# Optimization experiments

Hardware: AMD Instinct MI355X
Metric: run time of the kernel (lower is better)

The kernel has to match this reference:

```python
import jax, jax.numpy as jnp
import numpy as np

B, IDF, CDF, IH, IW, SRC = 32, 1024, 1024, 48, 48, 256


def setup_inputs() -> dict:
    key = jax.random.key(0)
    k1, k2, k3, k4 = jax.random.split(key, 4)
    inp = {
        "input": jax.random.normal(k1, (B, IDF, IH, IW), dtype=jnp.float32),
        "context": jax.random.normal(k2, (B, CDF, SRC), dtype=jnp.float32),
        "mask": jax.random.randint(k3, (B, SRC), 0, 2).astype(bool) & jax.random.randint(k4, (B, SRC), 0, 2).astype(bool),
        "W": jax.random.normal(jax.random.fold_in(key, 7), (IDF, CDF), dtype=jnp.float32) * 0.02,
    }
    return inp


def reference(input, context, mask, W):
    b, idf, ih, iw = input.shape
    q = ih * iw
    s = context.shape[2]
    # conv1x1(cdf->idf) on context: pure channel matmul
    sourceT = jnp.einsum("ic,bcs->bis", W, context)            # [B, idf, S]
    target = input.reshape(b, idf, q)                            # [B, idf, Q]
    attn = jnp.einsum("biq,bis->bqs", target, sourceT)          # [B, Q, S]
    attn_flat = attn.reshape(b * q, s)
    # faithful to original: mask.repeat(queryL, 1) tiles batch-major mask
    # onto batch-major-flattened rows -> row i uses mask[i % B]
    mask_full = jnp.tile(mask, (q, 1))                           # [Q*B, S] == [B*Q, S]
    attn_flat = jnp.where(mask_full, -jnp.inf, attn_flat)
    attn_flat = jax.nn.softmax(attn_flat, axis=-1)
    attn = attn_flat.reshape(b, q, s)
    attnT = jnp.transpose(attn, (0, 2, 1))                       # [B, S, Q]
    weightedContext = jnp.einsum("bis,bsq->biq", sourceT, attnT)
    weightedContext = weightedContext.reshape(b, idf, ih, iw)
    attn_out = attnT.reshape(b, s, ih, iw)
    return weightedContext, attn_out
```

## Files before the change

### kernel.cpp

```cpp
#include <hip/hip_runtime.h>

#define Bn  32
#define IDF 1024
#define CDF 1024
#define Qn  2304
#define Sn  256

typedef _Float16 f16;
typedef _Float16 f16x2 __attribute__((ext_vector_type(2)));
typedef _Float16 f16x4 __attribute__((ext_vector_type(4)));
typedef _Float16 f16x8 __attribute__((ext_vector_type(8)));
typedef float    f32x4 __attribute__((ext_vector_type(4)));

__device__ __forceinline__ void gll16(const void* g, void* l) {
    __builtin_amdgcn_global_load_lds((const __attribute__((address_space(1))) void*)g,
                                     (__attribute__((address_space(3))) void*)l, 16, 0, 0);
}

__device__ __forceinline__ void fsplit(float x, f16& hi, f16& lo) {
    hi = (f16)x;
    lo = (f16)(x - (float)hi);
}

__global__ __launch_bounds__(256) void k_wsplit(const float* __restrict__ W,
                                                f16* __restrict__ Wh, f16* __restrict__ Wl) {
    const int idx = (blockIdx.x * 256 + threadIdx.x) * 4;
    const float4 v = *reinterpret_cast<const float4*>(&W[idx]);
    f16x4 h4, l4;
    f16 h, l;
    fsplit(v.x, h, l); h4[0] = h; l4[0] = l;
    fsplit(v.y, h, l); h4[1] = h; l4[1] = l;
    fsplit(v.z, h, l); h4[2] = h; l4[2] = l;
    fsplit(v.w, h, l); h4[3] = h; l4[3] = l;
    *reinterpret_cast<f16x4*>(&Wh[idx]) = h4;
    *reinterpret_cast<f16x4*>(&Wl[idx]) = l4;
}

__global__ __launch_bounds__(256) void k_srcT(const f16* __restrict__ Wh,
                                              const f16* __restrict__ Wl,
                                              const float* __restrict__ ctx,
                                              f16* __restrict__ si_h, f16* __restrict__ si_l,
                                              f16* __restrict__ is_h, f16* __restrict__ is_l) {
    __shared__ alignas(16) char smem[49152];
    const int tid = threadIdx.x;
    const int w = tid >> 6, lane = tid & 63, g = lane >> 4, l15 = lane & 15;
    const int rxor = ((l15 >> 1) & 3) << 4;

    const int lin = (blockIdx.z * 8 + blockIdx.y) * 2 + blockIdx.x;
    const int swz = (lin & 7) * 64 + (lin >> 3);
    const int b = swz >> 4, rr = swz & 15;
    const int i0 = (rr >> 1) * 128, s0 = (rr & 1) * 128;

    const float* Cp = ctx + (size_t)b * CDF * Sn + s0;
    const int sl = tid & 127, ch = tid >> 7;
    const int swzw = ((sl >> 1) & 3) << 4;

    f32x4 acc[2][8];
    {
        f32x4 z = {0.f, 0.f, 0.f, 0.f};
        #pragma unroll
        for (int mf = 0; mf < 2; ++mf)
            #pragma unroll
            for (int nf = 0; nf < 8; ++nf)
                acc[mf][nf] = z;
    }

    #pragma unroll
    for (int part = 0; part < 2; ++part) {
        const int byt = w * 2048 + part * 1024 + lane * 16;
        const int rw = byt >> 6;
        const int co = ((((byt >> 4) & 3) ^ ((rw >> 1) & 3)) << 3);
        const size_t go = (size_t)(i0 + rw) * CDF + co;
        gll16(Wh + go, smem + w * 2048 + part * 1024);
        gll16(Wl + go, smem + 8192 + w * 2048 + part * 1024);
    }
    {
        float cv[16];
        #pragma unroll
        for (int j = 0; j < 16; ++j)
            cv[j] = Cp[(size_t)(ch * 16 + j) * Sn + sl];
        f16x8 h0, h1, l0, l1;
        #pragma unroll
        for (int j = 0; j < 8; ++j) { f16 h, l; fsplit(cv[j], h, l); h0[j] = h; l0[j] = l; }
        #pragma unroll
        for (int j = 0; j < 8; ++j) { f16 h, l; fsplit(cv[8 + j], h, l); h1[j] = h; l1[j] = l; }
        char* cb = smem + 16384 + sl * 64;
        *reinterpret_cast<f16x8*>(cb + (((ch * 32) + 0) ^ swzw))        = h0;
        *reinterpret_cast<f16x8*>(cb + (((ch * 32) + 16) ^ swzw))       = h1;
        *reinterpret_cast<f16x8*>(cb + 8192 + (((ch * 32) + 0) ^ swzw)) = l0;
        *reinterpret_cast<f16x8*>(cb + 8192 + (((ch * 32) + 16) ^ swzw))= l1;
    }
    __syncthreads();

    for (int t = 0; t < 32; ++t) {
        const int kk = t * 32;
        f16x8 fwh[2], fwl[2];
        #pragma unroll
        for (int mf = 0; mf < 2; ++mf) {
            const int row = w * 32 + mf * 16 + l15;
            fwh[mf] = *reinterpret_cast<const f16x8*>(smem + row * 64 + ((g * 16) ^ rxor));
            fwl[mf] = *reinterpret_cast<const f16x8*>(smem + 8192 + row * 64 + ((g * 16) ^ rxor));
        }
        asm volatile("s_waitcnt lgkmcnt(0)" ::: "memory");
        __builtin_amdgcn_sched_barrier(0);
        float cv[16];
        if (t < 31) {
            #pragma unroll
            for (int part = 0; part < 2; ++part) {
                const int byt = w * 2048 + part * 1024 + lane * 16;
                const int rw = byt >> 6;
                const int co = ((((byt >> 4) & 3) ^ ((rw >> 1) & 3)) << 3);
                const size_t go = (size_t)(i0 + rw) * CDF + kk + 32 + co;
                gll16(Wh + go, smem + w * 2048 + part * 1024);
                gll16(Wl + go, smem + 8192 + w * 2048 + part * 1024);
            }
            #pragma unroll
            for (int j = 0; j < 16; ++j)
                cv[j] = Cp[(size_t)(kk + 32 + ch * 16 + j) * Sn + sl];
        }
        const char* cbuf = smem + 16384 + (t & 1) * 16384;
        __builtin_amdgcn_s_setprio(1);
        #pragma unroll
        for (int nf = 0; nf < 8; ++nf) {
            const int srow = nf * 16 + l15;
            const f16x8 fch = *reinterpret_cast<const f16x8*>(cbuf + srow * 64 + ((g * 16) ^ rxor));
            const f16x8 fcl = *reinterpret_cast<const f16x8*>(cbuf + 8192 + srow * 64 + ((g * 16) ^ rxor));
            #pragma unroll
            for (int mf = 0; mf < 2; ++mf) {
                acc[mf][nf] = __builtin_amdgcn_mfma_f32_16x16x32_f16(fwh[mf], fch, acc[mf][nf], 0, 0, 0);
                acc[mf][nf] = __builtin_amdgcn_mfma_f32_16x16x32_f16(fwh[mf], fcl, acc[mf][nf], 0, 0, 0);
                acc[mf][nf] = __builtin_amdgcn_mfma_f32_16x16x32_f16(fwl[mf], fch, acc[mf][nf], 0, 0, 0);
            }
        }
        __builtin_amdgcn_s_setprio(0);
        if (t < 31) {
            f16x8 h0, h1, l0, l1;
            #pragma unroll
            for (int j = 0; j < 8; ++j) { f16 h, l; fsplit(cv[j], h, l); h0[j] = h; l0[j] = l; }
            #pragma unroll
            for (int j = 0; j < 8; ++j) { f16 h, l; fsplit(cv[8 + j], h, l); h1[j] = h; l1[j] = l; }
            char* cb = smem + 16384 + ((t + 1) & 1) * 16384 + sl * 64;
            *reinterpret_cast<f16x8*>(cb + (((ch * 32) + 0) ^ swzw))        = h0;
            *reinterpret_cast<f16x8*>(cb + (((ch * 32) + 16) ^ swzw))       = h1;
            *reinterpret_cast<f16x8*>(cb + 8192 + (((ch * 32) + 0) ^ swzw)) = l0;
            *reinterpret_cast<f16x8*>(cb + 8192 + (((ch * 32) + 16) ^ swzw))= l1;
        }
        __syncthreads();
    }

    #pragma unroll
    for (int mf = 0; mf < 2; ++mf)
        #pragma unroll
        for (int nf = 0; nf < 8; ++nf) {
            f16x4 h4, l4;
            #pragma unroll
            for (int r = 0; r < 4; ++r) { f16 h, l; fsplit(acc[mf][nf][r], h, l); h4[r] = h; l4[r] = l; }
            const int s  = s0 + nf * 16 + l15;
            const int ib = i0 + w * 32 + mf * 16 + g * 4;
            const size_t so = ((size_t)b * Sn + s) * IDF + ib;
            *reinterpret_cast<f16x4*>(&si_h[so]) = h4;
            *reinterpret_cast<f16x4*>(&si_l[so]) = l4;
        }

    #pragma unroll
    for (int p = 0; p < 2; ++p) {
        __syncthreads();
        #pragma unroll
        for (int mf = 0; mf < 2; ++mf) {
            const int ibase = w * 32 + mf * 16 + g * 4;
            #pragma unroll
            for (int nf4 = 0; nf4 < 4; ++nf4) {
                const int sl2 = nf4 * 16 + l15;
                #pragma unroll
                for (int r = 0; r < 4; ++r) {
                    const int row = ibase + r;
                    const int byo = (sl2 * 2) ^ ((row & 7) << 4);
                    f16 h, l; fsplit(acc[mf][p * 4 + nf4][r], h, l);
                    *reinterpret_cast<f16*>(smem + row * 128 + byo) = h;
                    *reinterpret_cast<f16*>(smem + 16384 + row * 128 + byo) = l;
                }
            }
        }
        __syncthreads();
        #pragma unroll
        for (int k = 0; k < 4; ++k) {
            const int c = tid + 256 * k;
            const int row = c >> 3, sc = (c & 7) * 8;
            const int byo = (sc * 2) ^ ((row & 7) << 4);
            const f16x8 vh = *reinterpret_cast<const f16x8*>(smem + row * 128 + byo);
            const f16x8 vl = *reinterpret_cast<const f16x8*>(smem + 16384 + row * 128 + byo);
            const size_t o = ((size_t)b * IDF + i0 + row) * Sn + s0 + p * 64 + sc;
            *reinterpret_cast<f16x8*>(&is_h[o]) = vh;
            *reinterpret_cast<f16x8*>(&is_l[o]) = vl;
        }
    }
}

__global__ __launch_bounds__(256) void k_attn(const float* __restrict__ inp,
                                              const f16* __restrict__ si_h,
                                              const f16* __restrict__ si_l,
                                              const int* __restrict__ mask,
                                              float* __restrict__ out1,
                                              f16* __restrict__ Ph) {
    __shared__ alignas(16) char smem[49152];
    const int tid = threadIdx.x;
    const int w = tid >> 6, lane = tid & 63, g = lane >> 4, l15 = lane & 15;
    const int rxor = ((l15 >> 1) & 3) << 4;
    const int awz  = ((lane >> 1) & 3) << 4;

    const int lin = blockIdx.y * 36 + blockIdx.x;
    const int swzb = (lin & 7) * 144 + (lin >> 3);
    const int b = swzb / 36, qt = swzb - b * 36;
    const int q0 = qt * 64;

    const float* Ap = inp + (size_t)b * IDF * Qn + q0;
    const f16* BhG = si_h + (size_t)b * Sn * IDF;
    const f16* BlG = si_l + (size_t)b * Sn * IDF;

    f32x4 acc[4][4];
    {
        f32x4 z = {0.f, 0.f, 0.f, 0.f};
        #pragma unroll
        for (int mf = 0; mf < 4; ++mf)
            #pragma unroll
            for (int nf = 0; nf < 4; ++nf)
                acc[mf][nf] = z;
    }

    #pragma unroll
    for (int it = 0; it < 4; ++it) {
        const int byt = w * 4096 + it * 1024 + lane * 16;
        const int s = byt >> 6;
        const int ko = ((((byt >> 4) & 3) ^ ((s >> 1) & 3)) << 3);
        const size_t go = (size_t)s * IDF + ko;
        gll16(BhG + go, smem + 16384 + w * 4096 + it * 1024);
        gll16(BlG + go, smem + 32768 + w * 4096 + it * 1024);
    }
    {
        float av[8];
        #pragma unroll
        for (int j = 0; j < 8; ++j)
            av[j] = Ap[(size_t)(w * 8 + j) * Qn + lane];
        f16x8 ah, al;
        #pragma unroll
        for (int j = 0; j < 8; ++j) { f16 h, lo; fsplit(av[j], h, lo); ah[j] = h; al[j] = lo; }
        *reinterpret_cast<f16x8*>(smem + lane * 64 + ((w * 16) ^ awz)) = ah;
        *reinterpret_cast<f16x8*>(smem + 4096 + lane * 64 + ((w * 16) ^ awz)) = al;
    }
    __syncthreads();

    for (int t = 0; t < 32; ++t) {
        const int kk = t * 32;
        f16x8 fbh[4], fbl[4];
        #pragma unroll
        for (int nf = 0; nf < 4; ++nf) {
            const int row = w * 64 + nf * 16 + l15;
            fbh[nf] = *reinterpret_cast<const f16x8*>(smem + 16384 + row * 64 + ((g * 16) ^ rxor));
            fbl[nf] = *reinterpret_cast<const f16x8*>(smem + 32768 + row * 64 + ((g * 16) ^ rxor));
        }
        asm volatile("s_waitcnt lgkmcnt(0)" ::: "memory");
        __builtin_amdgcn_sched_barrier(0);
        float av[8];
        if (t < 31) {
            #pragma unroll
            for (int it = 0; it < 4; ++it) {
                const int byt = w * 4096 + it * 1024 + lane * 16;
                const int s = byt >> 6;
                const int ko = ((((byt >> 4) & 3) ^ ((s >> 1) & 3)) << 3);
                const size_t go = (size_t)s * IDF + kk + 32 + ko;
                gll16(BhG + go, smem + 16384 + w * 4096 + it * 1024);
                gll16(BlG + go, smem + 32768 + w * 4096 + it * 1024);
            }
            #pragma unroll
            for (int j = 0; j < 8; ++j)
                av[j] = Ap[(size_t)(kk + 32 + w * 8 + j) * Qn + lane];
        }
        const char* ab = smem + (t & 1) * 8192;
        __builtin_amdgcn_s_setprio(1);
        #pragma unroll
        for (int mf = 0; mf < 4; ++mf) {
            const f16x8 fah = *reinterpret_cast<const f16x8*>(ab + (mf * 16 + l15) * 64 + ((g * 16) ^ rxor));
            const f16x8 fal = *reinterpret_cast<const f16x8*>(ab + 4096 + (mf * 16 + l15) * 64 + ((g * 16) ^ rxor));
            #pragma unroll
            for (int nf = 0; nf < 4; ++nf) {
                acc[mf][nf] = __builtin_amdgcn_mfma_f32_16x16x32_f16(fah, fbh[nf], acc[mf][nf], 0, 0, 0);
                acc[mf][nf] = __builtin_amdgcn_mfma_f32_16x16x32_f16(fah, fbl[nf], acc[mf][nf], 0, 0, 0);
                acc[mf][nf] = __builtin_amdgcn_mfma_f32_16x16x32_f16(fal, fbh[nf], acc[mf][nf], 0, 0, 0);
            }
        }
        __builtin_amdgcn_s_setprio(0);
        if (t < 31) {
            f16x8 ah, al;
            #pragma unroll
            for (int j = 0; j < 8; ++j) { f16 h, lo; fsplit(av[j], h, lo); ah[j] = h; al[j] = lo; }
            char* wb = smem + ((t + 1) & 1) * 8192;
            *reinterpret_cast<f16x8*>(wb + lane * 64 + ((w * 16) ^ awz)) = ah;
            *reinterpret_cast<f16x8*>(wb + 4096 + lane * 64 + ((w * 16) ^ awz)) = al;
        }
        __syncthreads();
    }

    int mv[2][4][4];
    #pragma unroll
    for (int h2 = 0; h2 < 2; ++h2)
        #pragma unroll
        for (int r = 0; r < 4; ++r)
            #pragma unroll
            for (int nf = 0; nf < 4; ++nf)
                mv[h2][r][nf] = mask[(h2 * 16 + g * 4 + r) * Sn + w * 64 + nf * 16 + l15];

    float* redm = reinterpret_cast<float*>(smem + 34816);
    float* reds = reinterpret_cast<float*>(smem + 35840);

    float mx[4][4], sm[4][4];
    #pragma unroll
    for (int mf = 0; mf < 4; ++mf)
        #pragma unroll
        for (int r = 0; r < 4; ++r) {
            float m = -3.0e38f;
            #pragma unroll
            for (int nf = 0; nf < 4; ++nf)
                if (!mv[mf & 1][r][nf]) m = fmaxf(m, acc[mf][nf][r]);
            m = fmaxf(m, __shfl_xor(m, 1, 64));
            m = fmaxf(m, __shfl_xor(m, 2, 64));
            m = fmaxf(m, __shfl_xor(m, 4, 64));
            m = fmaxf(m, __shfl_xor(m, 8, 64));
            mx[mf][r] = m;
        }
    if (l15 == 0) {
        #pragma unroll
        for (int mf = 0; mf < 4; ++mf)
            #pragma unroll
            for (int r = 0; r < 4; ++r)
                redm[w * 64 + mf * 16 + g * 4 + r] = mx[mf][r];
    }
    __syncthreads();
    #pragma unroll
    for (int mf = 0; mf < 4; ++mf)
        #pragma unroll
        for (int r = 0; r < 4; ++r) {
            const int q = mf * 16 + g * 4 + r;
            const float gm = fmaxf(fmaxf(redm[q], redm[64 + q]), fmaxf(redm[128 + q], redm[192 + q]));
            float ssum = 0.f;
            #pragma unroll
            for (int nf = 0; nf < 4; ++nf) {
                const float p = mv[mf & 1][r][nf] ? 0.f : __expf(acc[mf][nf][r] - gm);
                acc[mf][nf][r] = p;
                ssum += p;
            }
            ssum += __shfl_xor(ssum, 1, 64);
            ssum += __shfl_xor(ssum, 2, 64);
            ssum += __shfl_xor(ssum, 4, 64);
            ssum += __shfl_xor(ssum, 8, 64);
            sm[mf][r] = ssum;
        }
    if (l15 == 0) {
        #pragma unroll
        for (int mf = 0; mf < 4; ++mf)
            #pragma unroll
            for (int r = 0; r < 4; ++r)
                reds[w * 64 + mf * 16 + g * 4 + r] = sm[mf][r];
    }
    __syncthreads();
    #pragma unroll
    for (int mf = 0; mf < 4; ++mf)
        #pragma unroll
        for (int r = 0; r < 4; ++r) {
            const int q = mf * 16 + g * 4 + r;
            const float inv = 1.0f / (reds[q] + reds[64 + q] + reds[128 + q] + reds[192 + q]);
            #pragma unroll
            for (int nf = 0; nf < 4; ++nf)
                acc[mf][nf][r] *= inv;
        }

    float* Pl = reinterpret_cast<float*>(smem);
    float* O1 = out1 + (size_t)b * Sn * Qn + q0;
    f16* PhB = Ph + ((size_t)b * Qn + q0) * Sn;
    #pragma unroll
    for (int hf = 0; hf < 2; ++hf) {
        __syncthreads();
        if ((w >> 1) == hf) {
            #pragma unroll
            for (int mf = 0; mf < 4; ++mf)
                #pragma unroll
                for (int nf = 0; nf < 4; ++nf)
                    *reinterpret_cast<f32x4*>(
                        &Pl[((w & 1) * 64 + nf * 16 + l15) * 68 + mf * 16 + g * 4]) = acc[mf][nf];
        }
        __syncthreads();
        #pragma unroll
        for (int j = 0; j < 8; ++j) {
            const int sr = (tid >> 4) + j * 16;
            const int u  = (tid & 15) * 4;
            const f32x4 v = *reinterpret_cast<const f32x4*>(&Pl[sr * 68 + u]);
            *reinterpret_cast<f32x4*>(&O1[(size_t)(hf * 128 + sr) * Qn + u]) = v;
        }
        #pragma unroll
        for (int j = 0; j < 16; ++j) {
            const int colU = l15 + 16 * (j & 3);
            const int q    = (w * 4 + g) + 16 * (j >> 2);
            const float p0 = Pl[(2 * colU) * 68 + q];
            const float p1 = Pl[(2 * colU + 1) * 68 + q];
            f16x2 hh; hh[0] = (f16)p0; hh[1] = (f16)p1;
            *reinterpret_cast<f16x2*>(&PhB[(size_t)q * Sn + hf * 128 + 2 * colU]) = hh;
        }
    }
}

__global__ __launch_bounds__(256) void k_wc(const f16* __restrict__ is_h,
                                            const f16* __restrict__ is_l,
                                            const f16* __restrict__ Ph,
                                            float* __restrict__ out0) {
    __shared__ alignas(16) char smem[49152];
    const int tid = threadIdx.x;
    const int w = tid >> 6, lane = tid & 63, g = lane >> 4, l15 = lane & 15;
    const int wi = w >> 1, wq = w & 1;
    const int rxor = ((l15 >> 1) & 3) << 4;

    const int lin = (blockIdx.z * 8 + blockIdx.y) * 18 + blockIdx.x;
    const int swz = (lin & 7) * 576 + (lin >> 3);
    const int b = swz / 144;
    const int rr = swz - b * 144;
    const int it = rr / 18, qt = rr - it * 18;
    const int i0 = it * 128, q0 = qt * 128;

    const f16* AhG = is_h + ((size_t)b * IDF + i0) * Sn;
    const f16* AlG = is_l + ((size_t)b * IDF + i0) * Sn;
    const f16* BG  = Ph  + ((size_t)b * Qn + q0) * Sn;

    f32x4 acc[4][4];
    {
        f32x4 z = {0.f, 0.f, 0.f, 0.f};
        #pragma unroll
        for (int mf = 0; mf < 4; ++mf)
            #pragma unroll
            for (int nf = 0; nf < 4; ++nf)
                acc[mf][nf] = z;
    }

    #pragma unroll
    for (int t2 = 0; t2 < 2; ++t2) {
        const int byt = (w * 2 + t2) * 1024 + lane * 16;
        const int rw = byt >> 6;
        const int so = ((((byt >> 4) & 3) ^ ((rw >> 1) & 3)) << 3);
        const size_t go = (size_t)rw * Sn + so;
        gll16(AhG + go, smem + (w * 2 + t2) * 1024);
        gll16(AlG + go, smem + 8192 + (w * 2 + t2) * 1024);
        gll16(BG  + go, smem + 16384 + (w * 2 + t2) * 1024);
    }
    __syncthreads();

    for (int t = 0; t < 8; ++t) {
        const int kk = t * 32;
        if (t < 7) {
            #pragma unroll
            for (int t2 = 0; t2 < 2; ++t2) {
                const int byt = (w * 2 + t2) * 1024 + lane * 16;
                const int rw = byt >> 6;
                const int so = ((((byt >> 4) & 3) ^ ((rw >> 1) & 3)) << 3);
                const size_t go = (size_t)rw * Sn + kk + 32 + so;
                char* dst = smem + ((t + 1) & 1) * 24576 + (w * 2 + t2) * 1024;
                gll16(AhG + go, dst);
                gll16(AlG + go, dst + 8192);
                gll16(BG  + go, dst + 16384);
            }
        }
        const char* buf = smem + (t & 1) * 24576;
        f16x8 fah[4], fal[4];
        #pragma unroll
        for (int mf = 0; mf < 4; ++mf) {
            const int row = wi * 64 + mf * 16 + l15;
            fah[mf] = *reinterpret_cast<const f16x8*>(buf + row * 64 + ((g * 16) ^ rxor));
            fal[mf] = *reinterpret_cast<const f16x8*>(buf + 8192 + row * 64 + ((g * 16) ^ rxor));
        }
        __builtin_amdgcn_s_setprio(1);
        #pragma unroll
        for (int nf = 0; nf < 4; ++nf) {
            const int row = wq * 64 + nf * 16 + l15;
            const f16x8 fbh = *reinterpret_cast<const f16x8*>(buf + 16384 + row * 64 + ((g * 16) ^ rxor));
            #pragma unroll
            for (int mf = 0; mf < 4; ++mf) {
                acc[mf][nf] = __builtin_amdgcn_mfma_f32_16x16x32_f16(fah[mf], fbh, acc[mf][nf], 0, 0, 0);
                acc[mf][nf] = __builtin_amdgcn_mfma_f32_16x16x32_f16(fal[mf], fbh, acc[mf][nf], 0, 0, 0);
            }
        }
        __builtin_amdgcn_s_setprio(0);
        __syncthreads();
    }
    float* O = out0 + ((size_t)b * IDF + i0 + wi * 64) * Qn + q0 + wq * 64;
    #pragma unroll
    for (int mf = 0; mf < 4; ++mf)
        #pragma unroll
        for (int nf = 0; nf < 4; ++nf)
            #pragma unroll
            for (int r = 0; r < 4; ++r)
                O[(size_t)(mf * 16 + g * 4 + r) * Qn + nf * 16 + l15] = acc[mf][nf][r];
}

extern "C" void kernel_launch(void* const* d_in, const int* in_sizes, int n_in,
                              void* d_out, int out_size, void* d_ws, size_t ws_size,
                              hipStream_t stream) {
    const float* inp  = (const float*)d_in[0];
    const float* ctx  = (const float*)d_in[1];
    const int*   mask = (const int*)  d_in[2];
    const float* W    = (const float*)d_in[3];
    float* out0 = (float*)d_out;
    float* out1 = out0 + (size_t)Bn * IDF * Qn;

    char* ws = (char*)d_ws;
    const size_t SZ = (size_t)Bn * Sn * IDF * sizeof(f16);
    f16* si_h = (f16*)(ws);
    f16* si_l = (f16*)(ws + SZ);
    f16* is_h = (f16*)(ws + 2 * SZ);
    f16* is_l = (f16*)(ws + 3 * SZ);
    f16* Ph   = (f16*)(ws + 4 * SZ);
    f16* Wh   = (f16*)(ws + 4 * SZ);
    f16* Wl   = Wh + (size_t)IDF * CDF;

    hipLaunchKernelGGL(k_wsplit, dim3(IDF * CDF / 1024), dim3(256), 0, stream, W, Wh, Wl);
    hipLaunchKernelGGL(k_srcT, dim3(Sn / 128, IDF / 128, Bn), dim3(256), 0, stream,
                       Wh, Wl, ctx, si_h, si_l, is_h, is_l);
    hipLaunchKernelGGL(k_attn, dim3(Qn / 64, Bn), dim3(256), 0, stream,
                       inp, si_h, si_l, mask, out1, Ph);
    hipLaunchKernelGGL(k_wc, dim3(Qn / 128, IDF / 128, Bn), dim3(256), 0, stream,
                       is_h, is_l, Ph, out0);
}
```

Before: 396.0 us.

## Double query tile in attention kernel to reuse source tiles across more rows

Each attention block now covers 128 query positions instead of 64. Every staged tile of the split fp16 source matrix therefore feeds 8 MFMA row fragments instead of 4, halving global and LDS traffic for the source operand per query. The input load is restructured so 128 threads each split 16 channel values into hi/lo halves, with LDS grown to 64KB, launch bounds set to 2 blocks per CU, and the softmax reductions and epilogue writes re-indexed for the larger tile. The trade-offs are more accumulator registers, half as many blocks in the grid, and lower occupancy.

New measurement: 386.0 us. -2.5%, faster.

```diff
diff --git a/kernel.cpp b/kernel.cpp
--- a/kernel.cpp
+++ b/kernel.cpp
@@ -196,32 +196,34 @@
     }
 }
 
-__global__ __launch_bounds__(256) void k_attn(const float* __restrict__ inp,
-                                              const f16* __restrict__ si_h,
-                                              const f16* __restrict__ si_l,
-                                              const int* __restrict__ mask,
-                                              float* __restrict__ out1,
-                                              f16* __restrict__ Ph) {
-    __shared__ alignas(16) char smem[49152];
+__global__ __launch_bounds__(256, 2) void k_attn(const float* __restrict__ inp,
+                                                 const f16* __restrict__ si_h,
+                                                 const f16* __restrict__ si_l,
+                                                 const int* __restrict__ mask,
+                                                 float* __restrict__ out1,
+                                                 f16* __restrict__ Ph) {
+    __shared__ alignas(16) char smem[65536];
     const int tid = threadIdx.x;
     const int w = tid >> 6, lane = tid & 63, g = lane >> 4, l15 = lane & 15;
     const int rxor = ((l15 >> 1) & 3) << 4;
-    const int awz  = ((lane >> 1) & 3) << 4;
-
-    const int lin = blockIdx.y * 36 + blockIdx.x;
-    const int swzb = (lin & 7) * 144 + (lin >> 3);
-    const int b = swzb / 36, qt = swzb - b * 36;
-    const int q0 = qt * 64;
+
+    const int lin = blockIdx.y * 18 + blockIdx.x;
+    const int swzb = (lin & 7) * 72 + (lin >> 3);
+    const int b = swzb / 18, qt = swzb - b * 18;
+    const int q0 = qt * 128;
 
     const float* Ap = inp + (size_t)b * IDF * Qn + q0;
     const f16* BhG = si_h + (size_t)b * Sn * IDF;
     const f16* BlG = si_l + (size_t)b * Sn * IDF;
 
-    f32x4 acc[4][4];
+    const int sl = tid & 127, ch = tid >> 7;
+    const int swzw = ((sl >> 1) & 3) << 4;
+
+    f32x4 acc[8][4];
     {
         f32x4 z = {0.f, 0.f, 0.f, 0.f};
         #pragma unroll
-        for (int mf = 0; mf < 4; ++mf)
+        for (int mf = 0; mf < 8; ++mf)
             #pragma unroll
             for (int nf = 0; nf < 4; ++nf)
                 acc[mf][nf] = z;
@@ -233,19 +235,24 @@
         const int s = byt >> 6;
         const int ko = ((((byt >> 4) & 3) ^ ((s >> 1) & 3)) << 3);
         const size_t go = (size_t)s * IDF + ko;
-        gll16(BhG + go, smem + 16384 + w * 4096 + it * 1024);
-        gll16(BlG + go, smem + 32768 + w * 4096 + it * 1024);
+        gll16(BhG + go, smem + 32768 + w * 4096 + it * 1024);
+        gll16(BlG + go, smem + 49152 + w * 4096 + it * 1024);
     }
     {
-        float av[8];
-        #pragma unroll
-        for (int j = 0; j < 8; ++j)
-            av[j] = Ap[(size_t)(w * 8 + j) * Qn + lane];
-        f16x8 ah, al;
-        #pragma unroll
-        for (int j = 0; j < 8; ++j) { f16 h, lo; fsplit(av[j], h, lo); ah[j] = h; al[j] = lo; }
-        *reinterpret_cast<f16x8*>(smem + lane * 64 + ((w * 16) ^ awz)) = ah;
-        *reinterpret_cast<f16x8*>(smem + 4096 + lane * 64 + ((w * 16) ^ awz)) = al;
+        float cv[16];
+        #pragma unroll
+        for (int j = 0; j < 16; ++j)
+            cv[j] = Ap[(size_t)(ch * 16 + j) * Qn + sl];
+        f16x8 h0, h1, l0, l1;
+        #pragma unroll
+        for (int j = 0; j < 8; ++j) { f16 h, l; fsplit(cv[j], h, l); h0[j] = h; l0[j] = l; }
+        #pragma unroll
+        for (int j = 0; j < 8; ++j) { f16 h, l; fsplit(cv[8 + j], h, l); h1[j] = h; l1[j] = l; }
+        char* cb = smem + sl * 64;
+        *reinterpret_cast<f16x8*>(cb + (((ch * 32) + 0) ^ swzw))        = h0;
+        *reinterpret_cast<f16x8*>(cb + (((ch * 32) + 16) ^ swzw))       = h1;
+        *reinterpret_cast<f16x8*>(cb + 8192 + (((ch * 32) + 0) ^ swzw)) = l0;
+        *reinterpret_cast<f16x8*>(cb + 8192 + (((ch * 32) + 16) ^ swzw))= l1;
     }
     __syncthreads();
 
@@ -255,12 +262,12 @@
         #pragma unroll
         for (int nf = 0; nf < 4; ++nf) {
             const int row = w * 64 + nf * 16 + l15;
-            fbh[nf] = *reinterpret_cast<const f16x8*>(smem + 16384 + row * 64 + ((g * 16) ^ rxor));
-            fbl[nf] = *reinterpret_cast<const f16x8*>(smem + 32768 + row * 64 + ((g * 16) ^ rxor));
+            fbh[nf] = *reinterpret_cast<const f16x8*>(smem + 32768 + row * 64 + ((g * 16) ^ rxor));
+            fbl[nf] = *reinterpret_cast<const f16x8*>(smem + 49152 + row * 64 + ((g * 16) ^ rxor));
         }
         asm volatile("s_waitcnt lgkmcnt(0)" ::: "memory");
         __builtin_amdgcn_sched_barrier(0);
-        float av[8];
+        float cv[16];
         if (t < 31) {
             #pragma unroll
             for (int it = 0; it < 4; ++it) {
@@ -268,19 +275,19 @@
                 const int s = byt >> 6;
                 const int ko = ((((byt >> 4) & 3) ^ ((s >> 1) & 3)) << 3);
                 const size_t go = (size_t)s * IDF + kk + 32 + ko;
-                gll16(BhG + go, smem + 16384 + w * 4096 + it * 1024);
-                gll16(BlG + go, smem + 32768 + w * 4096 + it * 1024);
-            }
-            #pragma unroll
-            for (int j = 0; j < 8; ++j)
-                av[j] = Ap[(size_t)(kk + 32 + w * 8 + j) * Qn + lane];
-        }
-        const char* ab = smem + (t & 1) * 8192;
+                gll16(BhG + go, smem + 32768 + w * 4096 + it * 1024);
+                gll16(BlG + go, smem + 49152 + w * 4096 + it * 1024);
+            }
+            #pragma unroll
+            for (int j = 0; j < 16; ++j)
+                cv[j] = Ap[(size_t)(kk + 32 + ch * 16 + j) * Qn + sl];
+        }
+        const char* ab = smem + (t & 1) * 16384;
         __builtin_amdgcn_s_setprio(1);
         #pragma unroll
-        for (int mf = 0; mf < 4; ++mf) {
+        for (int mf = 0; mf < 8; ++mf) {
             const f16x8 fah = *reinterpret_cast<const f16x8*>(ab + (mf * 16 + l15) * 64 + ((g * 16) ^ rxor));
-            const f16x8 fal = *reinterpret_cast<const f16x8*>(ab + 4096 + (mf * 16 + l15) * 64 + ((g * 16) ^ rxor));
+            const f16x8 fal = *reinterpret_cast<const f16x8*>(ab + 8192 + (mf * 16 + l15) * 64 + ((g * 16) ^ rxor));
             #pragma unroll
             for (int nf = 0; nf < 4; ++nf) {
                 acc[mf][nf] = __builtin_amdgcn_mfma_f32_16x16x32_f16(fah, fbh[nf], acc[mf][nf], 0, 0, 0);
@@ -290,12 +297,16 @@
         }
         __builtin_amdgcn_s_setprio(0);
         if (t < 31) {
-            f16x8 ah, al;
-            #pragma unroll
-            for (int j = 0; j < 8; ++j) { f16 h, lo; fsplit(av[j], h, lo); ah[j] = h; al[j] = lo; }
-            char* wb = smem + ((t + 1) & 1) * 8192;
-            *reinterpret_cast<f16x8*>(wb + lane * 64 + ((w * 16) ^ awz)) = ah;
-            *reinterpret_cast<f16x8*>(wb + 4096 + lane * 64 + ((w * 16) ^ awz)) = al;
+            f16x8 h0, h1, l0, l1;
+            #pragma unroll
+            for (int j = 0; j < 8; ++j) { f16 h, l; fsplit(cv[j], h, l); h0[j] = h; l0[j] = l; }
+            #pragma unroll
+            for (int j = 0; j < 8; ++j) { f16 h, l; fsplit(cv[8 + j], h, l); h1[j] = h; l1[j] = l; }
+            char* cb = smem + ((t + 1) & 1) * 16384 + sl * 64;
+            *reinterpret_cast<f16x8*>(cb + (((ch * 32) + 0) ^ swzw))        = h0;
+            *reinterpret_cast<f16x8*>(cb + (((ch * 32) + 16) ^ swzw))       = h1;
+            *reinterpret_cast<f16x8*>(cb + 8192 + (((ch * 32) + 0) ^ swzw)) = l0;
+            *reinterpret_cast<f16x8*>(cb + 8192 + (((ch * 32) + 16) ^ swzw))= l1;
         }
         __syncthreads();
     }
@@ -310,11 +321,11 @@
                 mv[h2][r][nf] = mask[(h2 * 16 + g * 4 + r) * Sn + w * 64 + nf * 16 + l15];
 
     float* redm = reinterpret_cast<float*>(smem + 34816);
-    float* reds = reinterpret_cast<float*>(smem + 35840);
-
-    float mx[4][4], sm[4][4];
-    #pragma unroll
-    for (int mf = 0; mf < 4; ++mf)
+    float* reds = reinterpret_cast<float*>(smem + 36864);
+
+    float mx[8][4], sm[8][4];
+    #pragma unroll
+    for (int mf = 0; mf < 8; ++mf)
         #pragma unroll
         for (int r = 0; r < 4; ++r) {
             float m = -3.0e38f;
@@ -329,18 +340,18 @@
         }
     if (l15 == 0) {
         #pragma unroll
-        for (int mf = 0; mf < 4; ++mf)
+        for (int mf = 0; mf < 8; ++mf)
             #pragma unroll
             for (int r = 0; r < 4; ++r)
-                redm[w * 64 + mf * 16 + g * 4 + r] = mx[mf][r];
+                redm[w * 128 + mf * 16 + g * 4 + r] = mx[mf][r];
     }
     __syncthreads();
     #pragma unroll
-    for (int mf = 0; mf < 4; ++mf)
+    for (int mf = 0; mf < 8; ++mf)
         #pragma unroll
         for (int r = 0; r < 4; ++r) {
             const int q = mf * 16 + g * 4 + r;
-            const float gm = fmaxf(fmaxf(redm[q], redm[64 + q]), fmaxf(redm[128 + q], redm[192 + q]));
+            const float gm = fmaxf(fmaxf(redm[q], redm[128 + q]), fmaxf(redm[256 + q], redm[384 + q]));
             float ssum = 0.f;
             #pragma unroll
             for (int nf = 0; nf < 4; ++nf) {
@@ -356,18 +367,18 @@
         }
     if (l15 == 0) {
         #pragma unroll
-        for (int mf = 0; mf < 4; ++mf)
+        for (int mf = 0; mf < 8; ++mf)
             #pragma unroll
             for (int r = 0; r < 4; ++r)
-                reds[w * 64 + mf * 16 + g * 4 + r] = sm[mf][r];
+                reds[w * 128 + mf * 16 + g * 4 + r] = sm[mf][r];
     }
     __syncthreads();
     #pragma unroll
-    for (int mf = 0; mf < 4; ++mf)
+    for (int mf = 0; mf < 8; ++mf)
         #pragma unroll
         for (int r = 0; r < 4; ++r) {
             const int q = mf * 16 + g * 4 + r;
-            const float inv = 1.0f / (reds[q] + reds[64 + q] + reds[128 + q] + reds[192 + q]);
+            const float inv = 1.0f / (reds[q] + reds[128 + q] + reds[256 + q] + reds[384 + q]);
             #pragma unroll
             for (int nf = 0; nf < 4; ++nf)
                 acc[mf][nf][r] *= inv;
@@ -377,32 +388,32 @@
     float* O1 = out1 + (size_t)b * Sn * Qn + q0;
     f16* PhB = Ph + ((size_t)b * Qn + q0) * Sn;
     #pragma unroll
-    for (int hf = 0; hf < 2; ++hf) {
-        __syncthreads();
-        if ((w >> 1) == hf) {
-            #pragma unroll
-            for (int mf = 0; mf < 4; ++mf)
+    for (int p = 0; p < 4; ++p) {
+        __syncthreads();
+        if (w == p) {
+            #pragma unroll
+            for (int mf = 0; mf < 8; ++mf)
                 #pragma unroll
                 for (int nf = 0; nf < 4; ++nf)
                     *reinterpret_cast<f32x4*>(
-                        &Pl[((w & 1) * 64 + nf * 16 + l15) * 68 + mf * 16 + g * 4]) = acc[mf][nf];
+                        &Pl[(nf * 16 + l15) * 132 + mf * 16 + g * 4]) = acc[mf][nf];
         }
         __syncthreads();
         #pragma unroll
         for (int j = 0; j < 8; ++j) {
-            const int sr = (tid >> 4) + j * 16;
-            const int u  = (tid & 15) * 4;
-            const f32x4 v = *reinterpret_cast<const f32x4*>(&Pl[sr * 68 + u]);
-            *reinterpret_cast<f32x4*>(&O1[(size_t)(hf * 128 + sr) * Qn + u]) = v;
+            const int sr = (tid >> 5) + j * 8;
+            const int u  = (tid & 31) * 4;
+            const f32x4 v = *reinterpret_cast<const f32x4*>(&Pl[sr * 132 + u]);
+            *reinterpret_cast<f32x4*>(&O1[(size_t)(p * 64 + sr) * Qn + u]) = v;
         }
         #pragma unroll
         for (int j = 0; j < 16; ++j) {
-            const int colU = l15 + 16 * (j & 3);
-            const int q    = (w * 4 + g) + 16 * (j >> 2);
-            const float p0 = Pl[(2 * colU) * 68 + q];
-            const float p1 = Pl[(2 * colU + 1) * 68 + q];
+            const int colU = l15 + 16 * (j & 1);
+            const int q    = (w * 4 + g) + 16 * (j >> 1);
+            const float p0 = Pl[(2 * colU) * 132 + q];
+            const float p1 = Pl[(2 * colU + 1) * 132 + q];
             f16x2 hh; hh[0] = (f16)p0; hh[1] = (f16)p1;
-            *reinterpret_cast<f16x2*>(&PhB[(size_t)q * Sn + hf * 128 + 2 * colU]) = hh;
+            *reinterpret_cast<f16x2*>(&PhB[(size_t)q * Sn + p * 64 + 2 * colU]) = hh;
         }
     }
 }
@@ -520,7 +531,7 @@
     hipLaunchKernelGGL(k_wsplit, dim3(IDF * CDF / 1024), dim3(256), 0, stream, W, Wh, Wl);
     hipLaunchKernelGGL(k_srcT, dim3(Sn / 128, IDF / 128, Bn), dim3(256), 0, stream,
                        Wh, Wl, ctx, si_h, si_l, is_h, is_l);
-    hipLaunchKernelGGL(k_attn, dim3(Qn / 64, Bn), dim3(256), 0, stream,
+    hipLaunchKernelGGL(k_attn, dim3(Qn / 128, Bn), dim3(256), 0, stream,
                        inp, si_h, si_l, mask, out1, Ph);
     hipLaunchKernelGGL(k_wc, dim3(Qn / 128, IDF / 128, Bn), dim3(256), 0, stream,
                        is_h, is_l, Ph, out0);
```
